# Performance work log

Measured on AMD Instinct MI355X. Metric: run time of the kernel, lower is better.

Reference implementation:

```python
import jax, jax.numpy as jnp
import numpy as np

N_VISIBLE = 50000
N_HIDDEN = 5000
N_NODES = N_VISIBLE + N_HIDDEN
N_EDGES = 1_000_000
BATCH = 128


def setup_inputs() -> dict:
    key = jax.random.key(0)
    k1, k2, k3, k4, k5 = jax.random.split(key, 5)
    # parameters, initialized as in the torch module
    linear = 0.05 * (2.0 * jax.random.uniform(k1, (N_NODES,), dtype=jnp.float32) - 1.0)
    quadratic = 5.0 * (2.0 * jax.random.uniform(k2, (N_EDGES,), dtype=jnp.float32) - 1.0)
    # bipartite visible-hidden edges -> CSR-like flat buffers (via segment ids)
    flat_adj = jax.random.randint(k3, (N_EDGES,), 0, N_VISIBLE, dtype=jnp.int32).astype(jnp.int64)  # visible endpoint per edge
    seg_ids = jax.random.randint(k4, (N_EDGES,), 0, N_HIDDEN, dtype=jnp.int32).astype(jnp.int64)    # hidden bin per edge
    flat_j_idx = jnp.arange(N_EDGES, dtype=jnp.int64)  # quadratic coefficient index per flat entry
    hidden_idx = jnp.arange(N_HIDDEN, dtype=jnp.int64) + N_VISIBLE
    # observed spin configurations in {0,1} (mapped to +-1 inside reference)
    s = jax.random.randint(k5, (BATCH, N_NODES), 0, 2, dtype=jnp.int32)
    return {
        "linear": linear,
        "quadratic": quadratic,
        "s": s,
        "flat_adj": flat_adj,
        "flat_j_idx": flat_j_idx,
        "seg_ids": seg_ids,
        "hidden_idx": hidden_idx,
        "n_hidden": N_HIDDEN,
    }


def reference(linear, quadratic, s, flat_adj, flat_j_idx, seg_ids, hidden_idx, n_hidden):
    """Per-hidden-unit effective field + conditional spin expectation.

    eff[b, k] = linear[hidden_idx[k]]
                + sum_{e : seg_ids[e]==k} quadratic[flat_j_idx[e]] * s_pm[b, flat_adj[e]]
    returns tanh(-eff)  (conditional expectation of hidden spins given visibles)
    """
    s_pm = (2 * s - 1).astype(linear.dtype)                 # {0,1} -> {-1,+1}, (B, N)
    w = quadratic[flat_j_idx]                               # (E,)
    contrib = s_pm[:, flat_adj].T * w[:, None]              # (E, B) gathered neighbor terms
    field = jax.ops.segment_sum(contrib, seg_ids, num_segments=n_hidden)  # (K, B)
    eff = field.T + linear[hidden_idx][None, :]             # (B, K)
    return jnp.tanh(-eff)
```

## Files before the change

kernel.cpp:

```cpp
#include <hip/hip_runtime.h>
#include <math.h>
#include <stdint.h>

#define NV 50000
#define NH 5000
#define NN 55000
#define NCB 1250
#define NCBP 1280
#define BCAP 1280
#define KSLOT 384
#define CHUNK 4096


__device__ __forceinline__ uint32_t selmask(uint32_t word, uint32_t bsh) {
#if __has_builtin(__builtin_amdgcn_sbfe)
    return (uint32_t)__builtin_amdgcn_sbfe((int)word, bsh, 1u);
#else
    return (uint32_t)((int32_t)(word << (31u - bsh)) >> 31);
#endif
}

__global__ void __launch_bounds__(256) pack_zero_kernel(
        const int* __restrict__ s, uint32_t* __restrict__ bits,
        uint32_t* __restrict__ coarse_cnt) {
    if (blockIdx.x == 0)
        for (int i = threadIdx.x; i < NCB; i += 256) coarse_cnt[i] = 0u;
    int tid = blockIdx.x * 256 + threadIdx.x;
    int v = tid >> 2;
    int g = tid & 3;
    if (v >= NV) return;
    const int* col = s + (size_t)g * 32 * NN + v;
    uint32_t w = 0;
#pragma unroll
    for (int j = 0; j < 32; ++j)
        w |= (uint32_t)(col[(size_t)j * NN] & 1) << j;
    bits[(size_t)v * 4 + g] = w;
}

__global__ void __launch_bounds__(256) split_kernel(
        const int4* __restrict__ seg4, const int4* __restrict__ adj4,
        const float4* __restrict__ quad4,
        uint32_t* __restrict__ coarse_cnt, uint2* __restrict__ recs, int E) {
    __shared__ uint32_t hist[NCBP];
    __shared__ uint32_t curb[NCBP];
    __shared__ uint32_t gbase[NCBP];
    const int tid = threadIdx.x;
    for (int i = tid; i < NCBP; i += 256) { hist[i] = 0u; curb[i] = 0u; }
    __syncthreads();

    const int c0 = blockIdx.x * CHUNK;
    const int nloc = min(CHUNK, E - c0);
    const int t4max = (c0 + nloc) >> 2;
    int kreg[16];
#pragma unroll
    for (int j = 0; j < 4; ++j) {
        int t4 = (c0 >> 2) + j * 256 + tid;
        bool ok = t4 < t4max;
        int4 sg = ok ? seg4[t4] : make_int4(-1, -1, -1, -1);
        kreg[j * 4 + 0] = sg.x; kreg[j * 4 + 1] = sg.y;
        kreg[j * 4 + 2] = sg.z; kreg[j * 4 + 3] = sg.w;
        if (ok) {
            atomicAdd(&hist[sg.x >> 2], 1u);
            atomicAdd(&hist[sg.y >> 2], 1u);
            atomicAdd(&hist[sg.z >> 2], 1u);
            atomicAdd(&hist[sg.w >> 2], 1u);
        }
    }
    __syncthreads();
    for (int i = tid; i < NCB; i += 256) {
        uint32_t h = hist[i];
        if (h) gbase[i] = atomicAdd(&coarse_cnt[i], h);
    }
    __syncthreads();
#pragma unroll
    for (int j = 0; j < 4; ++j) {
        int t4 = (c0 >> 2) + j * 256 + tid;
        if (t4 < t4max) {
            int4 a = adj4[t4];
            float4 q = quad4[t4];
#pragma unroll
            for (int cmp = 0; cmp < 4; ++cmp) {
                int k = kreg[j * 4 + cmp];
                int v = (cmp == 0) ? a.x : (cmp == 1) ? a.y : (cmp == 2) ? a.z : a.w;
                float w = (cmp == 0) ? q.x : (cmp == 1) ? q.y : (cmp == 2) ? q.z : q.w;
                int bk = k >> 2;
                uint32_t rank = atomicAdd(&curb[bk], 1u);
                uint32_t pos = gbase[bk] + rank;
                if (pos < BCAP)
                    recs[(size_t)bk * BCAP + pos] =
                        make_uint2((uint32_t)v | ((uint32_t)(k & 3) << 16),
                                   __float_as_uint(w));
            }
        }
    }
}

__global__ void __launch_bounds__(256, 8) field_kernel(
        const uint32_t* __restrict__ coarse_cnt, const uint2* __restrict__ recs,
        const uint4* __restrict__ bits4, const float* __restrict__ linear,
        float* __restrict__ out) {
    const int x = blockIdx.x;
    const int bkt = (x & 7) * 157 + (x >> 3);
    if (bkt >= NCB) return;
    const int tid = threadIdx.x;

    __shared__ uint32_t cur2[2];
    __shared__ float swp[4][2];
    __shared__ __align__(16) uint32_t rows[2][5][KSLOT];
    __shared__ float part[2][256];

    const int cnt = (int)min(coarse_cnt[bkt], (uint32_t)BCAP);
    const uint2* __restrict__ region = recs + (size_t)bkt * BCAP;

    const int b = tid & 127;
    const int grp = tid >> 7;
    const uint32_t bsh = (uint32_t)(b & 31);
    const int widx = b >> 5;
    const int lane = tid & 63;
    const int wid = tid >> 6;

    for (int rnd = 0; rnd < 2; ++rnd) {
        if (tid < 2) cur2[tid] = 0u;
        __syncthreads();

        float s0 = 0.f, s1 = 0.f;
        for (int i = tid; i < cnt; i += 256) {
            uint2 r = region[i];
            int kl = (int)((r.x >> 16) & 3u);
            if ((kl >> 1) == rnd) {
                int kk = kl & 1;
                uint32_t p = atomicAdd(&cur2[kk], 1u);
                if (p < KSLOT) {
                    uint4 mw = bits4[r.x & 0xFFFFu];
                    rows[kk][0][p] = mw.x;
                    rows[kk][1][p] = mw.y;
                    rows[kk][2][p] = mw.z;
                    rows[kk][3][p] = mw.w;
                    rows[kk][4][p] = r.y;
                    float w = __uint_as_float(r.y);
                    if (kk == 0) s0 += w; else s1 += w;
                }
            }
        }
#pragma unroll
        for (int off = 32; off; off >>= 1) {
            s0 += __shfl_down(s0, off);
            s1 += __shfl_down(s1, off);
        }
        if (lane == 0) { swp[wid][0] = s0; swp[wid][1] = s1; }
        __syncthreads();

#pragma unroll
        for (int kk = 0; kk < 2; ++kk) {
            int c = min((int)cur2[kk], KSLOT);
            int T8 = (c + 7) & ~7;
            for (int t = c + tid; t < T8; t += 256) rows[kk][4][t] = 0u;
        }
        __syncthreads();

#pragma unroll
        for (int kk = 0; kk < 2; ++kk) {
            int T8k = (min((int)cur2[kk], KSLOT) + 7) & ~7;
            const uint32_t* mrow = rows[kk][widx];
            const uint32_t* wrow = rows[kk][4];
            float a0 = 0.f, a1 = 0.f, a2 = 0.f, a3 = 0.f;
            for (int i = grp * 4; i < T8k; i += 8) {
                uint4 mm = *(const uint4*)(mrow + i);
                uint4 ww = *(const uint4*)(wrow + i);
                a0 += __uint_as_float(ww.x & selmask(mm.x, bsh));
                a1 += __uint_as_float(ww.y & selmask(mm.y, bsh));
                a2 += __uint_as_float(ww.z & selmask(mm.z, bsh));
                a3 += __uint_as_float(ww.w & selmask(mm.w, bsh));
            }
            part[kk][tid] = (a0 + a1) + (a2 + a3);
        }
        __syncthreads();

        if (tid < 128) {
            int k0 = bkt * 4 + rnd * 2;
            float acc0 = part[0][tid] + part[0][tid + 128];
            float acc1 = part[1][tid] + part[1][tid + 128];
            float sum0 = swp[0][0] + swp[1][0] + swp[2][0] + swp[3][0];
            float sum1 = swp[0][1] + swp[1][1] + swp[2][1] + swp[3][1];
            float e0 = 2.f * acc0 - sum0 + linear[NV + k0];
            float e1 = 2.f * acc1 - sum1 + linear[NV + k0 + 1];
            float2 o = make_float2(tanhf(-e0), tanhf(-e1));
            *(float2*)(out + (size_t)tid * NH + k0) = o;
        }
        __syncthreads();
    }
}

extern "C" void kernel_launch(void* const* d_in, const int* in_sizes, int n_in,
                              void* d_out, int out_size, void* d_ws, size_t ws_size,
                              hipStream_t stream) {
    const float* linear = (const float*)d_in[0];
    const float* quad   = (const float*)d_in[1];
    const int*   s      = (const int*)d_in[2];
    const int*   adj    = (const int*)d_in[3];
    const int*   seg    = (const int*)d_in[5];
    const int E = in_sizes[5];
    float* out = (float*)d_out;

    char* ws = (char*)d_ws;
    uint32_t* bits       = (uint32_t*)(ws);
    uint32_t* coarse_cnt = (uint32_t*)(ws + 800000);
    uint2*    recs       = (uint2*)   (ws + 805120);

    pack_zero_kernel<<<(NV * 4 + 255) / 256, 256, 0, stream>>>(s, bits, coarse_cnt);
    const int nchunk = (E + CHUNK - 1) / CHUNK;
    split_kernel<<<nchunk, 256, 0, stream>>>(
        (const int4*)seg, (const int4*)adj, (const float4*)quad, coarse_cnt, recs, E);
    field_kernel<<<1256, 256, 0, stream>>>(coarse_cnt, recs, (const uint4*)bits,
                                           linear, out);
}
```

Before: 134.7 us.

## Use wave-aggregated slot allocation and 4-batch register tiling in field kernel

Replaces the per-record shared-memory atomic slot allocation with a wave-level ballot, popcount and single atomic per wave per hidden unit. It also remaps the accumulation so each thread handles four batch bits from one packed word across a quarter of the edges, for both hidden units at once. This reuses each LDS load of mask and weight four times and removes the serial two-unit loop. The cost is that each thread now covers fewer edges, so the per-thread tail work grows, and the padding changes to 16 entries with padded row strides.

```diff
diff --git a/kernel.cpp b/kernel.cpp
--- a/kernel.cpp
+++ b/kernel.cpp
@@ -9,6 +9,8 @@
 #define NCBP 1280
 #define BCAP 1280
 #define KSLOT 384
+#define KPAD 388
+#define PPAD 132
 #define CHUNK 4096
 
 
@@ -100,24 +102,27 @@
         const uint4* __restrict__ bits4, const float* __restrict__ linear,
         float* __restrict__ out) {
     const int x = blockIdx.x;
-    const int bkt = (x & 7) * 157 + (x >> 3);
-    if (bkt >= NCB) return;
+    const int blk = (x & 7) * 157 + (x >> 3);
+    if (blk >= NCB) return;
     const int tid = threadIdx.x;
+    const int lane = tid & 63;
+    const int wid = tid >> 6;
 
     __shared__ uint32_t cur2[2];
     __shared__ float swp[4][2];
-    __shared__ __align__(16) uint32_t rows[2][5][KSLOT];
-    __shared__ float part[2][256];
-
-    const int cnt = (int)min(coarse_cnt[bkt], (uint32_t)BCAP);
-    const uint2* __restrict__ region = recs + (size_t)bkt * BCAP;
-
-    const int b = tid & 127;
-    const int grp = tid >> 7;
-    const uint32_t bsh = (uint32_t)(b & 31);
-    const int widx = b >> 5;
-    const int lane = tid & 63;
-    const int wid = tid >> 6;
+    __shared__ __align__(16) uint32_t rows[2][5][KPAD];
+    __shared__ __align__(16) float part[2][4][PPAD];
+
+    const int cnt = (int)min(coarse_cnt[blk], (uint32_t)BCAP);
+    const uint2* __restrict__ region = recs + (size_t)blk * BCAP;
+
+    const int sub  = tid & 31;
+    const int gidx = tid >> 5;
+    const int akk  = gidx & 1;
+    const int g4   = gidx >> 1;
+    const int widx = sub >> 3;
+    const int nib  = sub & 7;
+    const uint32_t sh = (uint32_t)(nib * 4);
 
     for (int rnd = 0; rnd < 2; ++rnd) {
         if (tid < 2) cur2[tid] = 0u;
@@ -127,16 +132,32 @@
         for (int i = tid; i < cnt; i += 256) {
             uint2 r = region[i];
             int kl = (int)((r.x >> 16) & 3u);
-            if ((kl >> 1) == rnd) {
-                int kk = kl & 1;
-                uint32_t p = atomicAdd(&cur2[kk], 1u);
-                if (p < KSLOT) {
+            bool p = (kl >> 1) == rnd;
+            int kk = kl & 1;
+            uint64_t m0 = __ballot(p && kk == 0);
+            uint64_t m1 = __ballot(p && kk == 1);
+            uint32_t base0 = 0, base1 = 0;
+            if (m0) {
+                int l0 = __ffsll((unsigned long long)m0) - 1;
+                if (lane == l0) base0 = atomicAdd(&cur2[0], (uint32_t)__popcll(m0));
+                base0 = __shfl(base0, l0);
+            }
+            if (m1) {
+                int l1 = __ffsll((unsigned long long)m1) - 1;
+                if (lane == l1) base1 = atomicAdd(&cur2[1], (uint32_t)__popcll(m1));
+                base1 = __shfl(base1, l1);
+            }
+            if (p) {
+                uint64_t below = (1ull << lane) - 1ull;
+                uint32_t slot = kk ? base1 + (uint32_t)__popcll(m1 & below)
+                                   : base0 + (uint32_t)__popcll(m0 & below);
+                if (slot < KSLOT) {
                     uint4 mw = bits4[r.x & 0xFFFFu];
-                    rows[kk][0][p] = mw.x;
-                    rows[kk][1][p] = mw.y;
-                    rows[kk][2][p] = mw.z;
-                    rows[kk][3][p] = mw.w;
-                    rows[kk][4][p] = r.y;
+                    rows[kk][0][slot] = mw.x;
+                    rows[kk][1][slot] = mw.y;
+                    rows[kk][2][slot] = mw.z;
+                    rows[kk][3][slot] = mw.w;
+                    rows[kk][4][slot] = r.y;
                     float w = __uint_as_float(r.y);
                     if (kk == 0) s0 += w; else s1 += w;
                 }
@@ -150,42 +171,57 @@
         if (lane == 0) { swp[wid][0] = s0; swp[wid][1] = s1; }
         __syncthreads();
 
-#pragma unroll
-        for (int kk = 0; kk < 2; ++kk) {
-            int c = min((int)cur2[kk], KSLOT);
-            int T8 = (c + 7) & ~7;
-            for (int t = c + tid; t < T8; t += 256) rows[kk][4][t] = 0u;
-        }
-        __syncthreads();
-
-#pragma unroll
-        for (int kk = 0; kk < 2; ++kk) {
-            int T8k = (min((int)cur2[kk], KSLOT) + 7) & ~7;
-            const uint32_t* mrow = rows[kk][widx];
-            const uint32_t* wrow = rows[kk][4];
+        const int c0v = min((int)cur2[0], KSLOT);
+        const int c1v = min((int)cur2[1], KSLOT);
+        const int T0 = (c0v + 15) & ~15;
+        const int T1 = (c1v + 15) & ~15;
+        for (int t = c0v + tid; t < T0; t += 256) rows[0][4][t] = 0u;
+        for (int t = c1v + tid; t < T1; t += 256) rows[1][4][t] = 0u;
+        __syncthreads();
+
+        {
+            const int Tk = akk ? T1 : T0;
+            const uint32_t* __restrict__ mrow = rows[akk][widx];
+            const uint32_t* __restrict__ wrow = rows[akk][4];
             float a0 = 0.f, a1 = 0.f, a2 = 0.f, a3 = 0.f;
-            for (int i = grp * 4; i < T8k; i += 8) {
+            for (int i = g4 * 4; i < Tk; i += 16) {
                 uint4 mm = *(const uint4*)(mrow + i);
                 uint4 ww = *(const uint4*)(wrow + i);
-                a0 += __uint_as_float(ww.x & selmask(mm.x, bsh));
-                a1 += __uint_as_float(ww.y & selmask(mm.y, bsh));
-                a2 += __uint_as_float(ww.z & selmask(mm.z, bsh));
-                a3 += __uint_as_float(ww.w & selmask(mm.w, bsh));
-            }
-            part[kk][tid] = (a0 + a1) + (a2 + a3);
+                a0 += __uint_as_float(ww.x & selmask(mm.x, sh + 0u));
+                a1 += __uint_as_float(ww.x & selmask(mm.x, sh + 1u));
+                a2 += __uint_as_float(ww.x & selmask(mm.x, sh + 2u));
+                a3 += __uint_as_float(ww.x & selmask(mm.x, sh + 3u));
+                a0 += __uint_as_float(ww.y & selmask(mm.y, sh + 0u));
+                a1 += __uint_as_float(ww.y & selmask(mm.y, sh + 1u));
+                a2 += __uint_as_float(ww.y & selmask(mm.y, sh + 2u));
+                a3 += __uint_as_float(ww.y & selmask(mm.y, sh + 3u));
+                a0 += __uint_as_float(ww.z & selmask(mm.z, sh + 0u));
+                a1 += __uint_as_float(ww.z & selmask(mm.z, sh + 1u));
+                a2 += __uint_as_float(ww.z & selmask(mm.z, sh + 2u));
+                a3 += __uint_as_float(ww.z & selmask(mm.z, sh + 3u));
+                a0 += __uint_as_float(ww.w & selmask(mm.w, sh + 0u));
+                a1 += __uint_as_float(ww.w & selmask(mm.w, sh + 1u));
+                a2 += __uint_as_float(ww.w & selmask(mm.w, sh + 2u));
+                a3 += __uint_as_float(ww.w & selmask(mm.w, sh + 3u));
+            }
+            const int b4 = widx * 32 + nib * 4;
+            *(float4*)&part[akk][g4][b4] = make_float4(a0, a1, a2, a3);
         }
         __syncthreads();
 
         if (tid < 128) {
-            int k0 = bkt * 4 + rnd * 2;
-            float acc0 = part[0][tid] + part[0][tid + 128];
-            float acc1 = part[1][tid] + part[1][tid + 128];
-            float sum0 = swp[0][0] + swp[1][0] + swp[2][0] + swp[3][0];
-            float sum1 = swp[0][1] + swp[1][1] + swp[2][1] + swp[3][1];
+            const int b = tid;
+            float acc0 = (part[0][0][b] + part[0][1][b]) +
+                         (part[0][2][b] + part[0][3][b]);
+            float acc1 = (part[1][0][b] + part[1][1][b]) +
+                         (part[1][2][b] + part[1][3][b]);
+            int k0 = blk * 4 + rnd * 2;
+            float sum0 = (swp[0][0] + swp[1][0]) + (swp[2][0] + swp[3][0]);
+            float sum1 = (swp[0][1] + swp[1][1]) + (swp[2][1] + swp[3][1]);
             float e0 = 2.f * acc0 - sum0 + linear[NV + k0];
             float e1 = 2.f * acc1 - sum1 + linear[NV + k0 + 1];
             float2 o = make_float2(tanhf(-e0), tanhf(-e1));
-            *(float2*)(out + (size_t)tid * NH + k0) = o;
+            *(float2*)(out + (size_t)b * NH + k0) = o;
         }
         __syncthreads();
     }
```

After: 138.1 us. +2.5%, slower.

## Reuse histogram ranks in split and process four hidden units per pass

Applied to the files above, without the earlier changes.

The split kernel now keeps the rank returned by the histogram atomic, so the second atomic pass over a separate cursor array disappears. The field kernel drops its two-round loop and stages all four hidden units of a bucket into shared memory in one pass. That reads each record region once instead of twice, halves the barrier count, and writes a float4 per row. The cost is doubled shared memory, about 34KB per block, with occupancy lowered to 4 blocks per SM in the launch bounds.

```diff
diff --git a/kernel.cpp b/kernel.cpp
--- a/kernel.cpp
+++ b/kernel.cpp
@@ -42,16 +42,16 @@
         const float4* __restrict__ quad4,
         uint32_t* __restrict__ coarse_cnt, uint2* __restrict__ recs, int E) {
     __shared__ uint32_t hist[NCBP];
-    __shared__ uint32_t curb[NCBP];
     __shared__ uint32_t gbase[NCBP];
     const int tid = threadIdx.x;
-    for (int i = tid; i < NCBP; i += 256) { hist[i] = 0u; curb[i] = 0u; }
+    for (int i = tid; i < NCBP; i += 256) hist[i] = 0u;
     __syncthreads();
 
     const int c0 = blockIdx.x * CHUNK;
     const int nloc = min(CHUNK, E - c0);
     const int t4max = (c0 + nloc) >> 2;
     int kreg[16];
+    int rnk[16];
 #pragma unroll
     for (int j = 0; j < 4; ++j) {
         int t4 = (c0 >> 2) + j * 256 + tid;
@@ -60,10 +60,10 @@
         kreg[j * 4 + 0] = sg.x; kreg[j * 4 + 1] = sg.y;
         kreg[j * 4 + 2] = sg.z; kreg[j * 4 + 3] = sg.w;
         if (ok) {
-            atomicAdd(&hist[sg.x >> 2], 1u);
-            atomicAdd(&hist[sg.y >> 2], 1u);
-            atomicAdd(&hist[sg.z >> 2], 1u);
-            atomicAdd(&hist[sg.w >> 2], 1u);
+            rnk[j * 4 + 0] = (int)atomicAdd(&hist[sg.x >> 2], 1u);
+            rnk[j * 4 + 1] = (int)atomicAdd(&hist[sg.y >> 2], 1u);
+            rnk[j * 4 + 2] = (int)atomicAdd(&hist[sg.z >> 2], 1u);
+            rnk[j * 4 + 3] = (int)atomicAdd(&hist[sg.w >> 2], 1u);
         }
     }
     __syncthreads();
@@ -84,8 +84,7 @@
                 int v = (cmp == 0) ? a.x : (cmp == 1) ? a.y : (cmp == 2) ? a.z : a.w;
                 float w = (cmp == 0) ? q.x : (cmp == 1) ? q.y : (cmp == 2) ? q.z : q.w;
                 int bk = k >> 2;
-                uint32_t rank = atomicAdd(&curb[bk], 1u);
-                uint32_t pos = gbase[bk] + rank;
+                uint32_t pos = gbase[bk] + (uint32_t)rnk[j * 4 + cmp];
                 if (pos < BCAP)
                     recs[(size_t)bk * BCAP + pos] =
                         make_uint2((uint32_t)v | ((uint32_t)(k & 3) << 16),
@@ -95,99 +94,99 @@
     }
 }
 
-__global__ void __launch_bounds__(256, 8) field_kernel(
+__global__ void __launch_bounds__(256, 4) field_kernel(
         const uint32_t* __restrict__ coarse_cnt, const uint2* __restrict__ recs,
         const uint4* __restrict__ bits4, const float* __restrict__ linear,
         float* __restrict__ out) {
     const int x = blockIdx.x;
-    const int bkt = (x & 7) * 157 + (x >> 3);
-    if (bkt >= NCB) return;
+    const int blk = (x & 7) * 157 + (x >> 3);
+    if (blk >= NCB) return;
     const int tid = threadIdx.x;
-
-    __shared__ uint32_t cur2[2];
-    __shared__ float swp[4][2];
-    __shared__ __align__(16) uint32_t rows[2][5][KSLOT];
-    __shared__ float part[2][256];
-
-    const int cnt = (int)min(coarse_cnt[bkt], (uint32_t)BCAP);
-    const uint2* __restrict__ region = recs + (size_t)bkt * BCAP;
+    const int lane = tid & 63;
+    const int wid = tid >> 6;
+
+    __shared__ uint32_t cur4[4];
+    __shared__ float swp[4][4];
+    __shared__ __align__(16) uint32_t rows[4][5][KSLOT];
+    __shared__ float part[4][256];
+
+    if (tid < 4) cur4[tid] = 0u;
+    __syncthreads();
+
+    const int cnt = (int)min(coarse_cnt[blk], (uint32_t)BCAP);
+    const uint2* __restrict__ region = recs + (size_t)blk * BCAP;
+
+    float sw0 = 0.f, sw1 = 0.f, sw2 = 0.f, sw3 = 0.f;
+    for (int i = tid; i < cnt; i += 256) {
+        uint2 r = region[i];
+        int kl = (int)((r.x >> 16) & 3u);
+        uint32_t p = atomicAdd(&cur4[kl], 1u);
+        if (p < KSLOT) {
+            uint4 mw = bits4[r.x & 0xFFFFu];
+            rows[kl][0][p] = mw.x;
+            rows[kl][1][p] = mw.y;
+            rows[kl][2][p] = mw.z;
+            rows[kl][3][p] = mw.w;
+            rows[kl][4][p] = r.y;
+            float w = __uint_as_float(r.y);
+            if (kl == 0) sw0 += w; else if (kl == 1) sw1 += w;
+            else if (kl == 2) sw2 += w; else sw3 += w;
+        }
+    }
+#pragma unroll
+    for (int off = 32; off; off >>= 1) {
+        sw0 += __shfl_down(sw0, off);
+        sw1 += __shfl_down(sw1, off);
+        sw2 += __shfl_down(sw2, off);
+        sw3 += __shfl_down(sw3, off);
+    }
+    if (lane == 0) {
+        swp[wid][0] = sw0; swp[wid][1] = sw1;
+        swp[wid][2] = sw2; swp[wid][3] = sw3;
+    }
+    __syncthreads();
+
+#pragma unroll
+    for (int kl = 0; kl < 4; ++kl) {
+        int c = min((int)cur4[kl], KSLOT);
+        int T8 = (c + 7) & ~7;
+        for (int t = c + tid; t < T8; t += 256) rows[kl][4][t] = 0u;
+    }
+    __syncthreads();
 
     const int b = tid & 127;
     const int grp = tid >> 7;
     const uint32_t bsh = (uint32_t)(b & 31);
     const int widx = b >> 5;
-    const int lane = tid & 63;
-    const int wid = tid >> 6;
-
-    for (int rnd = 0; rnd < 2; ++rnd) {
-        if (tid < 2) cur2[tid] = 0u;
-        __syncthreads();
-
-        float s0 = 0.f, s1 = 0.f;
-        for (int i = tid; i < cnt; i += 256) {
-            uint2 r = region[i];
-            int kl = (int)((r.x >> 16) & 3u);
-            if ((kl >> 1) == rnd) {
-                int kk = kl & 1;
-                uint32_t p = atomicAdd(&cur2[kk], 1u);
-                if (p < KSLOT) {
-                    uint4 mw = bits4[r.x & 0xFFFFu];
-                    rows[kk][0][p] = mw.x;
-                    rows[kk][1][p] = mw.y;
-                    rows[kk][2][p] = mw.z;
-                    rows[kk][3][p] = mw.w;
-                    rows[kk][4][p] = r.y;
-                    float w = __uint_as_float(r.y);
-                    if (kk == 0) s0 += w; else s1 += w;
-                }
-            }
-        }
-#pragma unroll
-        for (int off = 32; off; off >>= 1) {
-            s0 += __shfl_down(s0, off);
-            s1 += __shfl_down(s1, off);
-        }
-        if (lane == 0) { swp[wid][0] = s0; swp[wid][1] = s1; }
-        __syncthreads();
-
-#pragma unroll
-        for (int kk = 0; kk < 2; ++kk) {
-            int c = min((int)cur2[kk], KSLOT);
-            int T8 = (c + 7) & ~7;
-            for (int t = c + tid; t < T8; t += 256) rows[kk][4][t] = 0u;
-        }
-        __syncthreads();
-
-#pragma unroll
-        for (int kk = 0; kk < 2; ++kk) {
-            int T8k = (min((int)cur2[kk], KSLOT) + 7) & ~7;
-            const uint32_t* mrow = rows[kk][widx];
-            const uint32_t* wrow = rows[kk][4];
-            float a0 = 0.f, a1 = 0.f, a2 = 0.f, a3 = 0.f;
-            for (int i = grp * 4; i < T8k; i += 8) {
-                uint4 mm = *(const uint4*)(mrow + i);
-                uint4 ww = *(const uint4*)(wrow + i);
-                a0 += __uint_as_float(ww.x & selmask(mm.x, bsh));
-                a1 += __uint_as_float(ww.y & selmask(mm.y, bsh));
-                a2 += __uint_as_float(ww.z & selmask(mm.z, bsh));
-                a3 += __uint_as_float(ww.w & selmask(mm.w, bsh));
-            }
-            part[kk][tid] = (a0 + a1) + (a2 + a3);
-        }
-        __syncthreads();
-
-        if (tid < 128) {
-            int k0 = bkt * 4 + rnd * 2;
-            float acc0 = part[0][tid] + part[0][tid + 128];
-            float acc1 = part[1][tid] + part[1][tid + 128];
-            float sum0 = swp[0][0] + swp[1][0] + swp[2][0] + swp[3][0];
-            float sum1 = swp[0][1] + swp[1][1] + swp[2][1] + swp[3][1];
-            float e0 = 2.f * acc0 - sum0 + linear[NV + k0];
-            float e1 = 2.f * acc1 - sum1 + linear[NV + k0 + 1];
-            float2 o = make_float2(tanhf(-e0), tanhf(-e1));
-            *(float2*)(out + (size_t)tid * NH + k0) = o;
-        }
-        __syncthreads();
+#pragma unroll
+    for (int kk = 0; kk < 4; ++kk) {
+        const int T8k = (min((int)cur4[kk], KSLOT) + 7) & ~7;
+        const uint32_t* __restrict__ mrow = rows[kk][widx];
+        const uint32_t* __restrict__ wrow = rows[kk][4];
+        float a0 = 0.f, a1 = 0.f, a2 = 0.f, a3 = 0.f;
+        for (int i = grp * 4; i < T8k; i += 8) {
+            uint4 mm = *(const uint4*)(mrow + i);
+            uint4 ww = *(const uint4*)(wrow + i);
+            a0 += __uint_as_float(ww.x & selmask(mm.x, bsh));
+            a1 += __uint_as_float(ww.y & selmask(mm.y, bsh));
+            a2 += __uint_as_float(ww.z & selmask(mm.z, bsh));
+            a3 += __uint_as_float(ww.w & selmask(mm.w, bsh));
+        }
+        part[kk][tid] = (a0 + a1) + (a2 + a3);
+    }
+    __syncthreads();
+
+    if (tid < 128) {
+        const int k0 = blk * 4;
+        float4 o;
+#pragma unroll
+        for (int kk = 0; kk < 4; ++kk) {
+            float acc = part[kk][tid] + part[kk][tid + 128];
+            float sum = (swp[0][kk] + swp[1][kk]) + (swp[2][kk] + swp[3][kk]);
+            float e = 2.f * acc - sum + linear[NV + k0 + kk];
+            (&o.x)[kk] = tanhf(-e);
+        }
+        *(float4*)(out + (size_t)tid * NH + k0) = o;
     }
 }
 
```

Result: slower. 146.5 us (+8.8%).
